# Kernel optimization log

Hardware: AMD Instinct MI355X
Metric: run time of the kernel (lower is better)

Reference implementation:

```python
import jax, jax.numpy as jnp
import numpy as np

SCALE = 1.0 / np.sqrt(128.0)  # 1/sqrt(head_size)
NEG = -1000000000.0


def setup_inputs() -> dict:
    key = jax.random.key(0)
    k1, k2, k3, k4 = jax.random.split(key, 4)
    B, H, S, D = 2, 16, 2048, 128
    q = jax.random.normal(k1, (B, H, S, D), dtype=jnp.float32)
    k = jax.random.normal(k2, (B, H, S, D), dtype=jnp.float32)
    v = jax.random.normal(k3, (B, H, S, D), dtype=jnp.float32)
    mask = jax.random.randint(k4, (B, S), 0, 2, dtype=jnp.int32)
    return {"q": q, "k": k, "v": v, "mask": mask}


def reference(q, k, v, mask):
    # scores: [B, H, Sq, Sk]
    scores = jnp.einsum("bhqd,bhkd->bhqk", q, k) * SCALE
    m = mask[:, None, None, :]  # [B,1,1,Sk], broadcast over heads and queries
    scores = jnp.where(m == 0, NEG, scores)
    weights = jax.nn.softmax(scores, axis=-1)
    out = jnp.einsum("bhqk,bhkd->bhqd", weights, v)
    return out
```

## Files before the change

### kernel.cpp

```cpp
#include <hip/hip_runtime.h>
#include <hip/hip_bf16.h>

typedef __attribute__((ext_vector_type(8))) short short8;
typedef __attribute__((ext_vector_type(4))) short short4v;
typedef __attribute__((ext_vector_type(4))) float floatx4;

#define NB 2
#define NH 16
#define NBH 32
#define SS 2048
#define DD 128
#define BQ 128
#define BK 32
#define KTILES (SS / BK)
#define SCALE 0.08838834764831845f
#define LOG2E 1.4426950408889634f
#define MAXB 12.0f
#define MASKED_BIAS -100000.0f

__device__ __forceinline__ short f2bf(float f) {
  union { float f; unsigned u; } x; x.f = f;
  return (short)((x.u + 0x7FFFu + ((x.u >> 16) & 1u)) >> 16);
}

__device__ __forceinline__ void pack8(short8* dst, float a, float b, float c, float d,
                                      float e, float f, float g, float h) {
  union { __hip_bfloat162 h2[4]; short8 v; } u;
  u.h2[0] = __float22bfloat162_rn(make_float2(a, b));
  u.h2[1] = __float22bfloat162_rn(make_float2(c, d));
  u.h2[2] = __float22bfloat162_rn(make_float2(e, f));
  u.h2[3] = __float22bfloat162_rn(make_float2(g, h));
  *dst = u.v;
}

__device__ __forceinline__ void gload_lds16(const short* g, short* l) {
  __builtin_amdgcn_global_load_lds(
      (const __attribute__((address_space(1))) void*)(g),
      (__attribute__((address_space(3))) void*)(l), 16, 0, 0);
}

__global__ __launch_bounds__(256) void prep_kernel(const float* __restrict__ k,
                                                   const float* __restrict__ v,
                                                   short* __restrict__ kbf,
                                                   short* __restrict__ vtg) {
  __shared__ short Ts[DD][68];
  const int kb = blockIdx.x, bh = blockIdx.y;
  const int tid = threadIdx.x;
  const size_t base = (size_t)bh * SS * DD + (size_t)(kb * 64) * DD;
  const float* kr = k + base;
  const float* vr = v + base;
  short* kw = kbf + base;
#pragma unroll
  for (int c = 0; c < 8; ++c) {
    int fi = c * 256 + tid;
    float4 a = ((const float4*)kr)[fi];
    short4v o;
    o[0] = f2bf(a.x); o[1] = f2bf(a.y); o[2] = f2bf(a.z); o[3] = f2bf(a.w);
    *(short4v*)(kw + (size_t)fi * 4) = o;
    float4 vv = ((const float4*)vr)[fi];
    int d0 = (fi * 4) & 127, key = (fi * 4) >> 7;
    Ts[d0 + 0][key] = f2bf(vv.x);
    Ts[d0 + 1][key] = f2bf(vv.y);
    Ts[d0 + 2][key] = f2bf(vv.z);
    Ts[d0 + 3][key] = f2bf(vv.w);
  }
  __syncthreads();
#pragma unroll
  for (int s = 0; s < 4; ++s) {
    int d = s * 32 + (tid >> 3);
    int c = tid & 7, kt2 = c >> 2, g = c & 3;
    short4v lo = *(short4v*)&Ts[d][kt2 * 32 + g * 4];
    short4v hi = *(short4v*)&Ts[d][kt2 * 32 + 16 + g * 4];
    short8 o;
#pragma unroll
    for (int r = 0; r < 4; ++r) { o[r] = lo[r]; o[4 + r] = hi[r]; }
    *(short8*)(vtg + ((size_t)(bh * DD + d)) * SS + (kb * 2 + kt2) * 32 + g * 8) = o;
  }
}

__global__ __launch_bounds__(256, 2) void fa_kernel(
    const float* __restrict__ q, const short* __restrict__ kbf,
    const short* __restrict__ vtg, const int* __restrict__ mask,
    float* __restrict__ out) {
  __shared__ __align__(16) short Ks[2][BK * DD];
  __shared__ __align__(16) short Vt[2][DD * BK];

  const int tid = threadIdx.x;
  const int wave = tid >> 6;
  const int lane = tid & 63;
  const int l16 = lane & 15;
  const int quad = lane >> 4;
  const int bh = blockIdx.y;
  const int b = bh >> 4;
  const int q0 = blockIdx.x * BQ;

  const size_t base = (size_t)bh * SS * DD;
  const float* qg = q + base;
  const short* kg = kbf + base;
  const short* vgb = vtg + (size_t)bh * DD * SS;
  const int4* mg4 = (const int4*)(mask + b * SS);
  const float c1 = SCALE * LOG2E, c2 = MAXB * LOG2E;

  short8 qf[2][4];
#pragma unroll
  for (int t = 0; t < 2; ++t) {
    const float* qp = qg + (size_t)(q0 + wave * 32 + t * 16 + l16) * DD;
#pragma unroll
    for (int dc = 0; dc < 4; ++dc) {
      float4 a = *(const float4*)(qp + dc * 32 + quad * 8);
      float4 bb = *(const float4*)(qp + dc * 32 + quad * 8 + 4);
      short8 tt;
      tt[0] = f2bf(a.x); tt[1] = f2bf(a.y); tt[2] = f2bf(a.z); tt[3] = f2bf(a.w);
      tt[4] = f2bf(bb.x); tt[5] = f2bf(bb.y); tt[6] = f2bf(bb.z); tt[7] = f2bf(bb.w);
      qf[t][dc] = tt;
    }
  }

  floatx4 Oacc[2][8];
#pragma unroll
  for (int t = 0; t < 2; ++t)
#pragma unroll
    for (int f = 0; f < 8; ++f) Oacc[t][f] = (floatx4){0.f, 0.f, 0.f, 0.f};
  float l_acc[2] = {0.f, 0.f};

  const short* kp[2];
  const short* vp[2];
#pragma unroll
  for (int i = 0; i < 2; ++i) {
    int c = wave * 2 + i;
    int krow = c * 4 + (lane >> 4);
    kp[i] = kg + (size_t)krow * DD + (((lane & 15) ^ (krow & 7)) * 8);
    int d = c * 16 + (lane >> 2);
    vp[i] = vgb + (size_t)d * SS + (((lane & 3) ^ ((lane >> 3) & 3)) * 8);
  }

  int koff[2];
#pragma unroll
  for (int nt = 0; nt < 2; ++nt) koff[nt] = (nt * 16 + l16) * DD;
  const int ksw = l16 & 7;
  const int voff = l16 * 32 + ((quad ^ ((l16 >> 1) & 3)) * 8);

#pragma unroll
  for (int i = 0; i < 2; ++i) {
    int c = wave * 2 + i;
    gload_lds16(kp[i], &Ks[0][c * 512]);
    gload_lds16(vp[i], &Vt[0][c * 512]);
    kp[i] += BK * DD;
    vp[i] += BK;
  }

#pragma unroll 2
  for (int kt = 0; kt < KTILES; ++kt) {
    const int cur = kt & 1;
    __syncthreads();
    if (kt + 1 < KTILES) {
#pragma unroll
      for (int i = 0; i < 2; ++i) {
        int c = wave * 2 + i;
        gload_lds16(kp[i], &Ks[cur ^ 1][c * 512]);
        gload_lds16(vp[i], &Vt[cur ^ 1][c * 512]);
        kp[i] += BK * DD;
        vp[i] += BK;
      }
    }
    int4 mm0 = mg4[kt * 8 + quad];
    int4 mm1 = mg4[kt * 8 + 4 + quad];

    floatx4 sacc[2][2];
#pragma unroll
    for (int t = 0; t < 2; ++t)
#pragma unroll
      for (int nt = 0; nt < 2; ++nt) sacc[t][nt] = (floatx4){0.f, 0.f, 0.f, 0.f};
#pragma unroll
    for (int nt = 0; nt < 2; ++nt)
#pragma unroll
      for (int dc = 0; dc < 4; ++dc) {
        short8 kf = *(const short8*)(&Ks[cur][0] + koff[nt] + (((dc * 4 + quad) ^ ksw) * 8));
        sacc[0][nt] = __builtin_amdgcn_mfma_f32_16x16x32_bf16(kf, qf[0][dc], sacc[0][nt], 0, 0, 0);
        sacc[1][nt] = __builtin_amdgcn_mfma_f32_16x16x32_bf16(kf, qf[1][dc], sacc[1][nt], 0, 0, 0);
      }

    float b0[4], b1[4];
    b0[0] = mm0.x ? -c2 : MASKED_BIAS;
    b0[1] = mm0.y ? -c2 : MASKED_BIAS;
    b0[2] = mm0.z ? -c2 : MASKED_BIAS;
    b0[3] = mm0.w ? -c2 : MASKED_BIAS;
    b1[0] = mm1.x ? -c2 : MASKED_BIAS;
    b1[1] = mm1.y ? -c2 : MASKED_BIAS;
    b1[2] = mm1.z ? -c2 : MASKED_BIAS;
    b1[3] = mm1.w ? -c2 : MASKED_BIAS;
    short8 pb[2];
#pragma unroll
    for (int t = 0; t < 2; ++t) {
      float e0 = __builtin_amdgcn_exp2f(fmaf(sacc[t][0][0], c1, b0[0]));
      float e1 = __builtin_amdgcn_exp2f(fmaf(sacc[t][0][1], c1, b0[1]));
      float e2 = __builtin_amdgcn_exp2f(fmaf(sacc[t][0][2], c1, b0[2]));
      float e3 = __builtin_amdgcn_exp2f(fmaf(sacc[t][0][3], c1, b0[3]));
      float g0 = __builtin_amdgcn_exp2f(fmaf(sacc[t][1][0], c1, b1[0]));
      float g1 = __builtin_amdgcn_exp2f(fmaf(sacc[t][1][1], c1, b1[1]));
      float g2 = __builtin_amdgcn_exp2f(fmaf(sacc[t][1][2], c1, b1[2]));
      float g3 = __builtin_amdgcn_exp2f(fmaf(sacc[t][1][3], c1, b1[3]));
      l_acc[t] += ((e0 + e1) + (e2 + e3)) + ((g0 + g1) + (g2 + g3));
      pack8(&pb[t], e0, e1, e2, e3, g0, g1, g2, g3);
    }

#pragma unroll
    for (int f = 0; f < 8; ++f) {
      short8 vv = *(const short8*)(&Vt[cur][0] + f * 512 + voff);
      Oacc[0][f] = __builtin_amdgcn_mfma_f32_16x16x32_bf16(vv, pb[0], Oacc[0][f], 0, 0, 0);
      Oacc[1][f] = __builtin_amdgcn_mfma_f32_16x16x32_bf16(vv, pb[1], Oacc[1][f], 0, 0, 0);
    }
  }

  float* og = out + base;
#pragma unroll
  for (int t = 0; t < 2; ++t) {
    float s = l_acc[t];
    s += __shfl_xor(s, 16);
    s += __shfl_xor(s, 32);
    float inv = 1.0f / s;
    float* orow = og + (size_t)(q0 + wave * 32 + t * 16 + l16) * DD + quad * 4;
#pragma unroll
    for (int f = 0; f < 8; ++f) {
      float4 w;
      w.x = Oacc[t][f][0] * inv;
      w.y = Oacc[t][f][1] * inv;
      w.z = Oacc[t][f][2] * inv;
      w.w = Oacc[t][f][3] * inv;
      *(float4*)(orow + f * 16) = w;
    }
  }
}

extern "C" void kernel_launch(void* const* d_in, const int* in_sizes, int n_in,
                              void* d_out, int out_size, void* d_ws, size_t ws_size,
                              hipStream_t stream) {
  const float* q = (const float*)d_in[0];
  const float* k = (const float*)d_in[1];
  const float* v = (const float*)d_in[2];
  const int* mask = (const int*)d_in[3];
  float* out = (float*)d_out;

  short* kbf = (short*)d_ws;
  short* vtg = kbf + (size_t)NBH * SS * DD;

  prep_kernel<<<dim3(SS / 64, NBH), dim3(256), 0, stream>>>(k, v, kbf, vtg);
  fa_kernel<<<dim3(SS / BQ, NBH), dim3(256), 0, stream>>>(q, kbf, vtg, mask, out);
}
```

Measured before the change: 218.8 us.

## Triple-buffer K/V tiles with explicit vmcnt waits and precompute mask bias in LDS

```diff
diff --git a/kernel.cpp b/kernel.cpp
--- a/kernel.cpp
+++ b/kernel.cpp
@@ -18,6 +18,10 @@
 #define MAXB 12.0f
 #define MASKED_BIAS -100000.0f
 
+#define WC_VM4 0x0F74
+#define WC_VM0 0x0F70
+#define WC_LGKM0 0xC07F
+
 __device__ __forceinline__ short f2bf(float f) {
   union { float f; unsigned u; } x; x.f = f;
   return (short)((x.u + 0x7FFFu + ((x.u >> 16) & 1u)) >> 16);
@@ -82,8 +86,9 @@
     const float* __restrict__ q, const short* __restrict__ kbf,
     const short* __restrict__ vtg, const int* __restrict__ mask,
     float* __restrict__ out) {
-  __shared__ __align__(16) short Ks[2][BK * DD];
-  __shared__ __align__(16) short Vt[2][DD * BK];
+  __shared__ __align__(16) short Ks[3][BK * DD];
+  __shared__ __align__(16) short Vt[3][DD * BK];
+  __shared__ float Bias[SS];
 
   const int tid = threadIdx.x;
   const int wave = tid >> 6;
@@ -98,7 +103,7 @@
   const float* qg = q + base;
   const short* kg = kbf + base;
   const short* vgb = vtg + (size_t)bh * DD * SS;
-  const int4* mg4 = (const int4*)(mask + b * SS);
+  const int* mg = mask + b * SS;
   const float c1 = SCALE * LOG2E, c2 = MAXB * LOG2E;
 
   short8 qf[2][4];
@@ -116,6 +121,19 @@
     }
   }
 
+  {
+    int i0 = tid * 8;
+    int4 m0 = *(const int4*)(mg + i0);
+    int4 m1 = *(const int4*)(mg + i0 + 4);
+    float4 f0, f1;
+    f0.x = m0.x ? -c2 : MASKED_BIAS; f0.y = m0.y ? -c2 : MASKED_BIAS;
+    f0.z = m0.z ? -c2 : MASKED_BIAS; f0.w = m0.w ? -c2 : MASKED_BIAS;
+    f1.x = m1.x ? -c2 : MASKED_BIAS; f1.y = m1.y ? -c2 : MASKED_BIAS;
+    f1.z = m1.z ? -c2 : MASKED_BIAS; f1.w = m1.w ? -c2 : MASKED_BIAS;
+    *(float4*)&Bias[i0] = f0;
+    *(float4*)&Bias[i0 + 4] = f1;
+  }
+
   floatx4 Oacc[2][8];
 #pragma unroll
   for (int t = 0; t < 2; ++t)
@@ -123,15 +141,18 @@
     for (int f = 0; f < 8; ++f) Oacc[t][f] = (floatx4){0.f, 0.f, 0.f, 0.f};
   float l_acc[2] = {0.f, 0.f};
 
-  const short* kp[2];
-  const short* vp[2];
+  const short* kpg[2];
+  const short* vpg[2];
+  int kls[2], vls[2];
 #pragma unroll
   for (int i = 0; i < 2; ++i) {
     int c = wave * 2 + i;
     int krow = c * 4 + (lane >> 4);
-    kp[i] = kg + (size_t)krow * DD + (((lane & 15) ^ (krow & 7)) * 8);
+    kpg[i] = kg + (size_t)krow * DD + (((lane & 15) ^ (krow & 7)) * 8);
     int d = c * 16 + (lane >> 2);
-    vp[i] = vgb + (size_t)d * SS + (((lane & 3) ^ ((lane >> 3) & 3)) * 8);
+    vpg[i] = vgb + (size_t)d * SS + (((lane & 3) ^ ((lane >> 3) & 3)) * 8);
+    kls[i] = c * 512;
+    vls[i] = c * 512;
   }
 
   int koff[2];
@@ -142,30 +163,39 @@
 
 #pragma unroll
   for (int i = 0; i < 2; ++i) {
-    int c = wave * 2 + i;
-    gload_lds16(kp[i], &Ks[0][c * 512]);
-    gload_lds16(vp[i], &Vt[0][c * 512]);
-    kp[i] += BK * DD;
-    vp[i] += BK;
-  }
-
-#pragma unroll 2
+    gload_lds16(kpg[i], &Ks[0][kls[i]]);
+    gload_lds16(vpg[i], &Vt[0][vls[i]]);
+  }
+#pragma unroll
+  for (int i = 0; i < 2; ++i) {
+    gload_lds16(kpg[i] + (size_t)BK * DD, &Ks[1][kls[i]]);
+    gload_lds16(vpg[i] + BK, &Vt[1][vls[i]]);
+  }
+  __builtin_amdgcn_s_waitcnt(WC_LGKM0);
+
+  int cur = 0;
+#pragma unroll 1
   for (int kt = 0; kt < KTILES; ++kt) {
-    const int cur = kt & 1;
-    __syncthreads();
-    if (kt + 1 < KTILES) {
+    if (kt + 1 < KTILES) __builtin_amdgcn_s_waitcnt(WC_VM4);
+    else                 __builtin_amdgcn_s_waitcnt(WC_VM0);
+    __builtin_amdgcn_s_barrier();
+
+    int ibuf = cur + 2; if (ibuf >= 3) ibuf -= 3;
+    if (kt + 2 < KTILES) {
+      const size_t kadv = (size_t)(kt + 2) * (BK * DD);
+      const int vadv = (kt + 2) * BK;
 #pragma unroll
       for (int i = 0; i < 2; ++i) {
-        int c = wave * 2 + i;
-        gload_lds16(kp[i], &Ks[cur ^ 1][c * 512]);
-        gload_lds16(vp[i], &Vt[cur ^ 1][c * 512]);
-        kp[i] += BK * DD;
-        vp[i] += BK;
+        gload_lds16(kpg[i] + kadv, &Ks[ibuf][kls[i]]);
+        gload_lds16(vpg[i] + vadv, &Vt[ibuf][vls[i]]);
       }
     }
-    int4 mm0 = mg4[kt * 8 + quad];
-    int4 mm1 = mg4[kt * 8 + 4 + quad];
-
+
+    float4 bb0 = *(const float4*)&Bias[kt * 32 + quad * 4];
+    float4 bb1 = *(const float4*)&Bias[kt * 32 + 16 + quad * 4];
+
+    const short* ksb = &Ks[cur][0];
+    const short* vsb = &Vt[cur][0];
     floatx4 sacc[2][2];
 #pragma unroll
     for (int t = 0; t < 2; ++t)
@@ -175,41 +205,34 @@
     for (int nt = 0; nt < 2; ++nt)
 #pragma unroll
       for (int dc = 0; dc < 4; ++dc) {
-        short8 kf = *(const short8*)(&Ks[cur][0] + koff[nt] + (((dc * 4 + quad) ^ ksw) * 8));
+        short8 kf = *(const short8*)(ksb + koff[nt] + (((dc * 4 + quad) ^ ksw) * 8));
         sacc[0][nt] = __builtin_amdgcn_mfma_f32_16x16x32_bf16(kf, qf[0][dc], sacc[0][nt], 0, 0, 0);
         sacc[1][nt] = __builtin_amdgcn_mfma_f32_16x16x32_bf16(kf, qf[1][dc], sacc[1][nt], 0, 0, 0);
       }
 
-    float b0[4], b1[4];
-    b0[0] = mm0.x ? -c2 : MASKED_BIAS;
-    b0[1] = mm0.y ? -c2 : MASKED_BIAS;
-    b0[2] = mm0.z ? -c2 : MASKED_BIAS;
-    b0[3] = mm0.w ? -c2 : MASKED_BIAS;
-    b1[0] = mm1.x ? -c2 : MASKED_BIAS;
-    b1[1] = mm1.y ? -c2 : MASKED_BIAS;
-    b1[2] = mm1.z ? -c2 : MASKED_BIAS;
-    b1[3] = mm1.w ? -c2 : MASKED_BIAS;
     short8 pb[2];
 #pragma unroll
     for (int t = 0; t < 2; ++t) {
-      float e0 = __builtin_amdgcn_exp2f(fmaf(sacc[t][0][0], c1, b0[0]));
-      float e1 = __builtin_amdgcn_exp2f(fmaf(sacc[t][0][1], c1, b0[1]));
-      float e2 = __builtin_amdgcn_exp2f(fmaf(sacc[t][0][2], c1, b0[2]));
-      float e3 = __builtin_amdgcn_exp2f(fmaf(sacc[t][0][3], c1, b0[3]));
-      float g0 = __builtin_amdgcn_exp2f(fmaf(sacc[t][1][0], c1, b1[0]));
-      float g1 = __builtin_amdgcn_exp2f(fmaf(sacc[t][1][1], c1, b1[1]));
-      float g2 = __builtin_amdgcn_exp2f(fmaf(sacc[t][1][2], c1, b1[2]));
-      float g3 = __builtin_amdgcn_exp2f(fmaf(sacc[t][1][3], c1, b1[3]));
+      float e0 = __builtin_amdgcn_exp2f(fmaf(sacc[t][0][0], c1, bb0.x));
+      float e1 = __builtin_amdgcn_exp2f(fmaf(sacc[t][0][1], c1, bb0.y));
+      float e2 = __builtin_amdgcn_exp2f(fmaf(sacc[t][0][2], c1, bb0.z));
+      float e3 = __builtin_amdgcn_exp2f(fmaf(sacc[t][0][3], c1, bb0.w));
+      float g0 = __builtin_amdgcn_exp2f(fmaf(sacc[t][1][0], c1, bb1.x));
+      float g1 = __builtin_amdgcn_exp2f(fmaf(sacc[t][1][1], c1, bb1.y));
+      float g2 = __builtin_amdgcn_exp2f(fmaf(sacc[t][1][2], c1, bb1.z));
+      float g3 = __builtin_amdgcn_exp2f(fmaf(sacc[t][1][3], c1, bb1.w));
       l_acc[t] += ((e0 + e1) + (e2 + e3)) + ((g0 + g1) + (g2 + g3));
       pack8(&pb[t], e0, e1, e2, e3, g0, g1, g2, g3);
     }
 
 #pragma unroll
     for (int f = 0; f < 8; ++f) {
-      short8 vv = *(const short8*)(&Vt[cur][0] + f * 512 + voff);
+      short8 vv = *(const short8*)(vsb + f * 512 + voff);
       Oacc[0][f] = __builtin_amdgcn_mfma_f32_16x16x32_bf16(vv, pb[0], Oacc[0][f], 0, 0, 0);
       Oacc[1][f] = __builtin_amdgcn_mfma_f32_16x16x32_bf16(vv, pb[1], Oacc[1][f], 0, 0, 0);
     }
+
+    cur = cur + 1; if (cur >= 3) cur = 0;
   }
 
   float* og = out + base;
```

Measured after the change: 211.9 us. 1.03x faster.
